# Kernel optimization log

Hardware: AMD Instinct MI355X
Metric: run time of the kernel (lower is better)

## Reference

```python
import jax, jax.numpy as jnp
import numpy as np

NUM_HEADS = 16
HEAD_DIM = 64
EMBED_DIM = 1024
NEG_INF = -1e9
LENGTHS = np.array([1024, 512, 768, 896, 1024, 640, 384, 896], dtype=np.int32)


def rotate_half(x):
    d = x.shape[-1] // 2
    return jnp.concatenate([-x[..., d:], x[..., :d]], axis=-1)


def setup_inputs() -> dict:
    key = jax.random.key(0)
    ks = jax.random.split(key, 8)
    E, H, Dh = EMBED_DIM, NUM_HEADS, HEAD_DIM
    T = int(LENGTHS.sum())  # 6144 packed tokens
    hidden_states = jax.random.normal(ks[0], (T, E), jnp.float32)
    # RoPE tables: positions restart at 0 for each packed segment
    pos = np.concatenate([np.arange(l) for l in LENGTHS]).astype(np.float32)
    inv_freq = 1.0 / (10000.0 ** (np.arange(0, Dh, 2, dtype=np.float32) / Dh))
    freqs = pos[:, None] * inv_freq[None, :]           # [T, Dh/2]
    emb = np.concatenate([freqs, freqs], axis=-1)       # [T, Dh]
    cos = jnp.asarray(np.cos(emb), jnp.float32)
    sin = jnp.asarray(np.sin(emb), jnp.float32)
    s = 0.02
    Wq = jax.random.normal(ks[1], (E, E), jnp.float32) * s
    Wk = jax.random.normal(ks[2], (E, E), jnp.float32) * s
    Wv = jax.random.normal(ks[3], (E, E), jnp.float32) * s
    Wo = jax.random.normal(ks[4], (E, E), jnp.float32) * s
    bq = jnp.zeros((E,), jnp.float32)
    bv = jnp.zeros((E,), jnp.float32)
    bo = jnp.zeros((E,), jnp.float32)
    return dict(hidden_states=hidden_states, seq_len=jnp.asarray(LENGTHS),
                cos=cos, sin=sin, Wq=Wq, bq=bq, Wk=Wk, Wv=Wv, bv=bv, Wo=Wo, bo=bo)


def reference(hidden_states, seq_len, cos, sin, Wq, bq, Wk, Wv, bv, Wo, bo):
    T, E = hidden_states.shape
    H, Dh = NUM_HEADS, HEAD_DIM
    # q/k/v projections (k_proj has no bias, matching nn.Linear(bias=False))
    q = (hidden_states @ Wq.T + bq).reshape(T, H, Dh)
    k = (hidden_states @ Wk.T).reshape(T, H, Dh)
    v = (hidden_states @ Wv.T + bv).reshape(T, H, Dh)
    # rotary embedding, cos/sin broadcast over heads
    c = cos[:, None, :]
    s = sin[:, None, :]
    q = q * c + rotate_half(q) * s
    k = k * c + rotate_half(k) * s
    # unpack ragged -> padded [B, Lmax, H, Dh] (indices are static wrt data)
    lens = np.asarray(seq_len)
    B = lens.shape[0]
    Lmax = int(lens.max())
    cu = np.concatenate([[0], np.cumsum(lens)])
    pad_idx = cu[:-1, None] + np.arange(Lmax)[None, :]   # [B, Lmax]
    valid = np.arange(Lmax)[None, :] < lens[:, None]     # [B, Lmax]
    pad_idx = np.where(valid, pad_idx, 0)
    qp = q[pad_idx]  # [B, Lmax, H, Dh]
    kp = k[pad_idx]
    vp = v[pad_idx]
    # attention with causal + key-padding mask (equivalent to per-segment loop)
    scores = jnp.einsum('bqhd,bkhd->bhqk', qp, kp) / np.sqrt(Dh).astype(np.float32)
    causal = np.tril(np.ones((Lmax, Lmax), dtype=bool))
    mask = causal[None, None, :, :] & valid[:, None, None, :]
    scores = jnp.where(mask, scores, NEG_INF)
    probs = jax.nn.softmax(scores, axis=-1)
    out = jnp.einsum('bhqk,bkhd->bqhd', probs, vp).reshape(B, Lmax, E)
    # repack padded -> [T, E]
    b_ids = np.repeat(np.arange(B), lens)
    l_ids = np.concatenate([np.arange(l) for l in lens])
    packed = out[b_ids, l_ids]
    return packed @ Wo.T + bo
```

## Files before the change

### kernel.cpp

```cpp
#include <hip/hip_runtime.h>
#include <stdint.h>

typedef __bf16 bf16;
typedef __bf16 bf16x8 __attribute__((ext_vector_type(8)));
typedef __bf16 bf16x4 __attribute__((ext_vector_type(4)));
typedef float f32x4 __attribute__((ext_vector_type(4)));

#define T_TOT 6144
#define E_DIM 1024
#define NHEAD 16

__device__ __forceinline__ void gload16(const void* g, void* l) {
    __builtin_amdgcn_global_load_lds((const __attribute__((address_space(1))) void*)g,
                                     (__attribute__((address_space(3))) void*)l, 16, 0, 0);
}

__global__ __launch_bounds__(256) void cvt_all_kernel(const float* __restrict__ hs,
        const float* __restrict__ wq, const float* __restrict__ wk,
        const float* __restrict__ wv, const float* __restrict__ wo,
        bf16* __restrict__ hsb, bf16* __restrict__ wqb, bf16* __restrict__ wkb,
        bf16* __restrict__ wvb, bf16* __restrict__ wob) {
    const size_t TE = (size_t)T_TOT * E_DIM;
    const size_t EE = (size_t)E_DIM * E_DIM;
    size_t i = ((size_t)blockIdx.x * 256 + threadIdx.x) * 4;
    const float* src; bf16* dst; size_t off;
    if (i < TE)               { src = hs; dst = hsb; off = i; }
    else if (i < TE + EE)     { src = wq; dst = wqb; off = i - TE; }
    else if (i < TE + 2 * EE) { src = wk; dst = wkb; off = i - TE - EE; }
    else if (i < TE + 3 * EE) { src = wv; dst = wvb; off = i - TE - 2 * EE; }
    else                      { src = wo; dst = wob; off = i - TE - 3 * EE; }
    float4 v = *reinterpret_cast<const float4*>(src + off);
    union { bf16 h[4]; uint2 u; } pk;
    pk.h[0] = (bf16)v.x; pk.h[1] = (bf16)v.y; pk.h[2] = (bf16)v.z; pk.h[3] = (bf16)v.w;
    *reinterpret_cast<uint2*>(dst + off) = pk.u;
}

__global__ __launch_bounds__(256, 2) void qkv_gemm_kernel(
        const bf16* __restrict__ hsb,
        const bf16* __restrict__ wq, const bf16* __restrict__ wk, const bf16* __restrict__ wv,
        const float* __restrict__ bq, const float* __restrict__ bv,
        const float* __restrict__ cosb, const float* __restrict__ sinb,
        bf16* __restrict__ qo, bf16* __restrict__ ko, bf16* __restrict__ vto) {
    __shared__ bf16 As[192 * 64];
    __shared__ bf16 Bs[128 * 64];

    const int b    = blockIdx.x;
    const int swzi = (b & 7) * 96 + (b >> 3);
    const int bn   = swzi & 7;
    const int t1   = swzi >> 3;
    const int bm   = t1 & 31;
    const int z    = t1 >> 5;
    const bf16*  W    = (z == 0) ? wq : (z == 1) ? wk : wv;
    const float* bias = (z == 0) ? bq : (z == 1) ? nullptr : bv;

    const int tid  = threadIdx.x;
    const int lane = tid & 63;
    const int wid  = tid >> 6;
    const int l15  = lane & 15, l4 = lane >> 4;
    const int wr   = wid >> 1, wc = wid & 1;

    f32x4 acc[6][4] = {};

    const bf16* Ag = hsb + (size_t)bm * 192 * E_DIM;
    const bf16* Bg = W   + (size_t)bn * 128 * E_DIM;

    const int srow = tid >> 3, sc8 = (tid & 7) * 8;

    for (int k0 = 0; k0 < E_DIM; k0 += 64) {
        #pragma unroll
        for (int j = 0; j < 6; ++j)
            gload16(Ag + (size_t)(j * 32 + srow) * E_DIM + k0 + sc8,
                    As + (size_t)(j * 256 + wid * 64) * 8);
        #pragma unroll
        for (int j = 0; j < 4; ++j)
            gload16(Bg + (size_t)(j * 32 + srow) * E_DIM + k0 + sc8,
                    Bs + (size_t)(j * 256 + wid * 64) * 8);
        __syncthreads();

        bf16x8 bfr[4][2];
        #pragma unroll
        for (int n = 0; n < 4; ++n)
            #pragma unroll
            for (int ks = 0; ks < 2; ++ks)
                bfr[n][ks] = *reinterpret_cast<const bf16x8*>(
                    &Bs[(wc * 64 + n * 16 + l15) * 64 + (ks * 4 + l4) * 8]);
        #pragma unroll
        for (int m = 0; m < 6; ++m) {
            bf16x8 af0 = *reinterpret_cast<const bf16x8*>(
                &As[(wr * 96 + m * 16 + l15) * 64 + l4 * 8]);
            bf16x8 af1 = *reinterpret_cast<const bf16x8*>(
                &As[(wr * 96 + m * 16 + l15) * 64 + (4 + l4) * 8]);
            #pragma unroll
            for (int n = 0; n < 4; ++n) {
                acc[m][n] = __builtin_amdgcn_mfma_f32_16x16x32_bf16(af0, bfr[n][0], acc[m][n], 0, 0, 0);
                acc[m][n] = __builtin_amdgcn_mfma_f32_16x16x32_bf16(af1, bfr[n][1], acc[m][n], 0, 0, 0);
            }
        }
        __syncthreads();
    }

    const int colb = bn * 128 + wc * 64;
    if (z <= 1) {
        bf16* out = (z == 0) ? qo : ko;
        #pragma unroll
        for (int n = 0; n < 2; ++n) {
            const int col_lo = colb + n * 16 + l15;
            const int dlo    = n * 16 + l15;
            const float b_lo = bias ? bias[col_lo] : 0.0f;
            const float b_hi = bias ? bias[col_lo + 32] : 0.0f;
            #pragma unroll
            for (int m = 0; m < 6; ++m) {
                #pragma unroll
                for (int r = 0; r < 4; ++r) {
                    const int t = bm * 192 + wr * 96 + m * 16 + l4 * 4 + r;
                    const float c = cosb[t * 64 + dlo];
                    const float s = sinb[t * 64 + dlo];
                    const float lo = acc[m][n][r] + b_lo;
                    const float hi = acc[m][n + 2][r] + b_hi;
                    out[(size_t)t * E_DIM + col_lo]      = (bf16)(lo * c - hi * s);
                    out[(size_t)t * E_DIM + col_lo + 32] = (bf16)(hi * c + lo * s);
                }
            }
        }
    } else {
        #pragma unroll
        for (int n = 0; n < 4; ++n) {
            const int col  = colb + n * 16 + l15;
            const float bc = bias[col];
            #pragma unroll
            for (int m = 0; m < 6; ++m) {
                const int t0r = bm * 192 + wr * 96 + m * 16 + l4 * 4;
                bf16x4 pk;
                #pragma unroll
                for (int r = 0; r < 4; ++r)
                    pk[r] = (bf16)(acc[m][n][r] + bc);
                *reinterpret_cast<bf16x4*>(vto + (size_t)col * T_TOT + t0r) = pk;
            }
        }
    }
}

__global__ __launch_bounds__(256, 4) void out_gemm_kernel(
        const bf16* __restrict__ attnb, const bf16* __restrict__ wo,
        const float* __restrict__ bo, float* __restrict__ out) {
    __shared__ bf16 As[64 * 64];
    __shared__ bf16 Bs[128 * 64];
    const int b   = blockIdx.x;
    const int swz = (b & 7) * 96 + (b >> 3);
    const int bn  = swz & 7;
    const int bm  = swz >> 3;

    const int tid  = threadIdx.x;
    const int lane = tid & 63;
    const int wid  = tid >> 6;
    const int l15  = lane & 15, l4 = lane >> 4;
    const int wr   = wid >> 1, wc = wid & 1;

    f32x4 acc[2][4] = {};

    const bf16* Ag = attnb + (size_t)bm * 64 * E_DIM;
    const bf16* Bg = wo    + (size_t)bn * 128 * E_DIM;

    const int srow = tid >> 3, sc8 = (tid & 7) * 8;

    for (int k0 = 0; k0 < E_DIM; k0 += 64) {
        #pragma unroll
        for (int j = 0; j < 2; ++j)
            gload16(Ag + (size_t)(j * 32 + srow) * E_DIM + k0 + sc8,
                    As + (size_t)(j * 256 + wid * 64) * 8);
        #pragma unroll
        for (int j = 0; j < 4; ++j)
            gload16(Bg + (size_t)(j * 32 + srow) * E_DIM + k0 + sc8,
                    Bs + (size_t)(j * 256 + wid * 64) * 8);
        __syncthreads();

        bf16x8 bfr[4][2];
        #pragma unroll
        for (int n = 0; n < 4; ++n)
            #pragma unroll
            for (int ks = 0; ks < 2; ++ks)
                bfr[n][ks] = *reinterpret_cast<const bf16x8*>(
                    &Bs[(wc * 64 + n * 16 + l15) * 64 + (ks * 4 + l4) * 8]);
        #pragma unroll
        for (int m = 0; m < 2; ++m) {
            bf16x8 af0 = *reinterpret_cast<const bf16x8*>(
                &As[(wr * 32 + m * 16 + l15) * 64 + l4 * 8]);
            bf16x8 af1 = *reinterpret_cast<const bf16x8*>(
                &As[(wr * 32 + m * 16 + l15) * 64 + (4 + l4) * 8]);
            #pragma unroll
            for (int n = 0; n < 4; ++n) {
                acc[m][n] = __builtin_amdgcn_mfma_f32_16x16x32_bf16(af0, bfr[n][0], acc[m][n], 0, 0, 0);
                acc[m][n] = __builtin_amdgcn_mfma_f32_16x16x32_bf16(af1, bfr[n][1], acc[m][n], 0, 0, 0);
            }
        }
        __syncthreads();
    }

    #pragma unroll
    for (int n = 0; n < 4; ++n) {
        const int col  = bn * 128 + wc * 64 + n * 16 + l15;
        const float bc = bo[col];
        #pragma unroll
        for (int m = 0; m < 2; ++m) {
            const int rowb = bm * 64 + wr * 32 + m * 16 + l4 * 4;
            #pragma unroll
            for (int r = 0; r < 4; ++r)
                out[(size_t)(rowb + r) * E_DIM + col] = acc[m][n][r] + bc;
        }
    }
}

__device__ const int g_pair_b[48] = {
    0,6,0,6,0,6,0,1,0,1,0,1,0,1,0,5,4,5,4,5,4,5,4,5,
    4,2,4,2,4,2,4,2,3,2,3,2,3,7,3,7,3,7,3,7,3,7,7,7};
__device__ const int g_pair_j[48] = {
    0,2,1,1,2,0,3,3,4,2,5,1,6,0,7,4,0,3,1,2,2,1,3,0,
    4,5,5,4,6,3,7,2,0,1,1,0,2,6,3,5,4,4,5,3,6,2,0,1};

__device__ __forceinline__ void stage_kv(const bf16* __restrict__ kp, const bf16* __restrict__ vtp,
                                         bf16* kls, bf16* vls, int tok0, int h,
                                         int wid, int lane) {
    #pragma unroll
    for (int j = 0; j < 2; ++j) {
        const int c   = j * 256 + wid * 64 + lane;
        const int row = c >> 3;
        const int c8s = (c & 7) ^ (row & 7);
        gload16(kp  + (size_t)(tok0 + row) * E_DIM + h * 64 + c8s * 8,
                kls + (size_t)(j * 256 + wid * 64) * 8);
        gload16(vtp + (size_t)(h * 64 + row) * T_TOT + tok0 + c8s * 8,
                vls + (size_t)(j * 256 + wid * 64) * 8);
    }
}

__device__ __forceinline__ int swz(int j, int col8) {
    return j * 64 + ((col8 ^ (j & 7)) << 3);
}

__global__ __launch_bounds__(256, 3) void attn_kernel(const bf16* __restrict__ q,
                                                      const bf16* __restrict__ k,
                                                      const bf16* __restrict__ vt,
                                                      bf16* __restrict__ attn) {
    const int cu[9] = {0, 1024, 1536, 2304, 3200, 4224, 4864, 5248, 6144};
    __shared__ bf16 kls[2][64 * 64];
    __shared__ bf16 vls[2][64 * 64];
    __shared__ bf16 p_lds[4][16][72];
    const int h   = blockIdx.x & 15;
    const int pid = blockIdx.x >> 4;
    const int tid = threadIdx.x, lane = tid & 63, wid = tid >> 6;
    const int l15 = lane & 15, l4 = lane >> 4;

    const int b   = g_pair_b[pid];
    const int jlo = g_pair_j[pid];
    const int nq  = (cu[b + 1] - cu[b]) >> 6;

    #pragma unroll 1
    for (int pass = 0; pass < 2; ++pass) {
        const int j   = pass ? (nq - 1 - jlo) : jlo;
        const int q0  = cu[b] + j * 64 + wid * 16;
        const int nkt = j + 1;
        const int pq  = j * 64 + wid * 16 + l15;

        bf16x8 qf[2];
        #pragma unroll
        for (int kk = 0; kk < 2; ++kk) {
            bf16x8 raw = *reinterpret_cast<const bf16x8*>(
                q + (size_t)(q0 + l15) * E_DIM + h * 64 + kk * 32 + l4 * 8);
            #pragma unroll
            for (int e = 0; e < 8; ++e)
                qf[kk][e] = (bf16)((float)raw[e] * 0.125f);
        }

        f32x4 o[4] = {};
        float mcur = -1e30f, lcur = 0.0f;

        stage_kv(k, vt, kls[0], vls[0], cu[b], h, wid, lane);
        __syncthreads();

        for (int kt = 0; kt < nkt; ++kt) {
            const int cur = kt & 1;
            if (kt + 1 < nkt)
                stage_kv(k, vt, kls[cur ^ 1], vls[cur ^ 1], cu[b] + (kt + 1) * 64, h, wid, lane);

            const int j0 = kt * 64;
            const bool diag = (kt == nkt - 1);

            f32x4 s[4] = {};
            #pragma unroll
            for (int nt = 0; nt < 4; ++nt) {
                #pragma unroll
                for (int kk = 0; kk < 2; ++kk) {
                    bf16x8 kf = *reinterpret_cast<const bf16x8*>(&kls[cur][swz(nt * 16 + l15, kk * 4 + l4)]);
                    s[nt] = __builtin_amdgcn_mfma_f32_16x16x32_bf16(kf, qf[kk], s[nt], 0, 0, 0);
                }
            }

            float tmax = -1e30f;
            #pragma unroll
            for (int nt = 0; nt < 4; ++nt) {
                #pragma unroll
                for (int r = 0; r < 4; ++r) {
                    float sv = s[nt][r];
                    if (diag) {
                        const int kp = j0 + nt * 16 + l4 * 4 + r;
                        sv = (kp <= pq) ? sv : -1e30f;
                    }
                    s[nt][r] = sv;
                    tmax = fmaxf(tmax, sv);
                }
            }
            tmax = fmaxf(tmax, __shfl_xor(tmax, 16));
            tmax = fmaxf(tmax, __shfl_xor(tmax, 32));

            if (!__all(tmax <= mcur + 8.0f)) {
                const float mnew  = fmaxf(mcur, tmax);
                const float alpha = __expf(mcur - mnew);
                #pragma unroll
                for (int nt = 0; nt < 4; ++nt)
                    #pragma unroll
                    for (int r = 0; r < 4; ++r) o[nt][r] *= alpha;
                lcur *= alpha;
                mcur = mnew;
            }

            float rs = 0.0f;
            #pragma unroll
            for (int nt = 0; nt < 4; ++nt) {
                bf16x4 pk;
                #pragma unroll
                for (int r = 0; r < 4; ++r) {
                    float p = __expf(s[nt][r] - mcur);
                    rs += p;
                    pk[r] = (bf16)p;
                }
                *reinterpret_cast<bf16x4*>(&p_lds[wid][l15][nt * 16 + l4 * 4]) = pk;
            }
            rs += __shfl_xor(rs, 16);
            rs += __shfl_xor(rs, 32);
            lcur += rs;

            bf16x8 pf[2];
            #pragma unroll
            for (int kk = 0; kk < 2; ++kk)
                pf[kk] = *reinterpret_cast<const bf16x8*>(&p_lds[wid][l15][kk * 32 + l4 * 8]);

            #pragma unroll
            for (int nt = 0; nt < 4; ++nt) {
                #pragma unroll
                for (int kk = 0; kk < 2; ++kk) {
                    bf16x8 vf = *reinterpret_cast<const bf16x8*>(&vls[cur][swz(nt * 16 + l15, kk * 4 + l4)]);
                    o[nt] = __builtin_amdgcn_mfma_f32_16x16x32_bf16(vf, pf[kk], o[nt], 0, 0, 0);
                }
            }
            __syncthreads();
        }

        const float rinv = __builtin_amdgcn_rcpf(lcur);
        #pragma unroll
        for (int nt = 0; nt < 4; ++nt) {
            bf16x4 pk;
            #pragma unroll
            for (int r = 0; r < 4; ++r)
                pk[r] = (bf16)(o[nt][r] * rinv);
            *reinterpret_cast<bf16x4*>(
                attn + (size_t)(q0 + l15) * E_DIM + h * 64 + nt * 16 + l4 * 4) = pk;
        }
    }
}

extern "C" void kernel_launch(void* const* d_in, const int* in_sizes, int n_in,
                              void* d_out, int out_size, void* d_ws, size_t ws_size,
                              hipStream_t stream) {
    const float* hs   = (const float*)d_in[0];
    const float* cosb = (const float*)d_in[2];
    const float* sinb = (const float*)d_in[3];
    const float* Wq   = (const float*)d_in[4];
    const float* bq   = (const float*)d_in[5];
    const float* Wk   = (const float*)d_in[6];
    const float* Wv   = (const float*)d_in[7];
    const float* bv   = (const float*)d_in[8];
    const float* Wo   = (const float*)d_in[9];
    const float* bo   = (const float*)d_in[10];

    const size_t TE = (size_t)T_TOT * E_DIM;
    const size_t EE = (size_t)E_DIM * E_DIM;

    char* w = (char*)d_ws;
    bf16* hsb   = (bf16*)w; w += TE * 2;
    bf16* wqb   = (bf16*)w; w += EE * 2;
    bf16* wkb   = (bf16*)w; w += EE * 2;
    bf16* wvb   = (bf16*)w; w += EE * 2;
    bf16* wob   = (bf16*)w; w += EE * 2;
    bf16* qb    = (bf16*)w; w += TE * 2;
    bf16* kb    = (bf16*)w; w += TE * 2;
    bf16* vtb   = (bf16*)w; w += TE * 2;
    bf16* attnb = (bf16*)w; w += TE * 2;

    const int cvt_blocks = (int)((TE + 4 * EE) / 4 / 256);
    cvt_all_kernel<<<cvt_blocks, 256, 0, stream>>>(hs, Wq, Wk, Wv, Wo, hsb, wqb, wkb, wvb, wob);

    qkv_gemm_kernel<<<768, 256, 0, stream>>>(hsb, wqb, wkb, wvb, bq, bv, cosb, sinb, qb, kb, vtb);

    attn_kernel<<<768, 256, 0, stream>>>(qb, kb, vtb, attnb);

    out_gemm_kernel<<<768, 256, 0, stream>>>(attnb, wob, bo, (float*)d_out);
}
```

Baseline: 113.0 us.

## Merge paired query tiles into one KV sweep sharing staged K/V tiles

Previously each block processed its low and high query tiles in two sequential passes, staging K/V tiles twice for the overlapping prefix. Now both query tiles are processed in a single loop over KV tiles up to the high tile. The low tile's MFMAs and softmax are predicated off once past its diagonal. This halves K/V staging and barrier count for the shared prefix, at the cost of doubled register state (two accumulators, two Q fragments) that may pressure occupancy under launch_bounds(256,3).

```diff
diff --git a/kernel.cpp b/kernel.cpp
--- a/kernel.cpp
+++ b/kernel.cpp
@@ -243,7 +243,8 @@
     const int cu[9] = {0, 1024, 1536, 2304, 3200, 4224, 4864, 5248, 6144};
     __shared__ bf16 kls[2][64 * 64];
     __shared__ bf16 vls[2][64 * 64];
-    __shared__ bf16 p_lds[4][16][72];
+    __shared__ bf16 pA_lds[4][16][72];
+    __shared__ bf16 pB_lds[4][16][72];
     const int h   = blockIdx.x & 15;
     const int pid = blockIdx.x >> 4;
     const int tid = threadIdx.x, lane = tid & 63, wid = tid >> 6;
@@ -252,118 +253,133 @@
     const int b   = g_pair_b[pid];
     const int jlo = g_pair_j[pid];
     const int nq  = (cu[b + 1] - cu[b]) >> 6;
-
-    #pragma unroll 1
-    for (int pass = 0; pass < 2; ++pass) {
-        const int j   = pass ? (nq - 1 - jlo) : jlo;
-        const int q0  = cu[b] + j * 64 + wid * 16;
-        const int nkt = j + 1;
-        const int pq  = j * 64 + wid * 16 + l15;
-
-        bf16x8 qf[2];
-        #pragma unroll
-        for (int kk = 0; kk < 2; ++kk) {
-            bf16x8 raw = *reinterpret_cast<const bf16x8*>(
-                q + (size_t)(q0 + l15) * E_DIM + h * 64 + kk * 32 + l4 * 8);
-            #pragma unroll
-            for (int e = 0; e < 8; ++e)
-                qf[kk][e] = (bf16)((float)raw[e] * 0.125f);
-        }
-
-        f32x4 o[4] = {};
-        float mcur = -1e30f, lcur = 0.0f;
-
-        stage_kv(k, vt, kls[0], vls[0], cu[b], h, wid, lane);
-        __syncthreads();
-
-        for (int kt = 0; kt < nkt; ++kt) {
-            const int cur = kt & 1;
-            if (kt + 1 < nkt)
-                stage_kv(k, vt, kls[cur ^ 1], vls[cur ^ 1], cu[b] + (kt + 1) * 64, h, wid, lane);
-
-            const int j0 = kt * 64;
-            const bool diag = (kt == nkt - 1);
-
-            f32x4 s[4] = {};
-            #pragma unroll
-            for (int nt = 0; nt < 4; ++nt) {
+    const int jhi = nq - 1 - jlo;
+
+    const int qA0 = cu[b] + jlo * 64 + wid * 16;
+    const int qB0 = cu[b] + jhi * 64 + wid * 16;
+    const int pqA = jlo * 64 + wid * 16 + l15;
+    const int pqB = jhi * 64 + wid * 16 + l15;
+
+    bf16x8 qfA[2], qfB[2];
+    #pragma unroll
+    for (int kk = 0; kk < 2; ++kk) {
+        bf16x8 ra = *reinterpret_cast<const bf16x8*>(
+            q + (size_t)(qA0 + l15) * E_DIM + h * 64 + kk * 32 + l4 * 8);
+        bf16x8 rb = *reinterpret_cast<const bf16x8*>(
+            q + (size_t)(qB0 + l15) * E_DIM + h * 64 + kk * 32 + l4 * 8);
+        #pragma unroll
+        for (int e = 0; e < 8; ++e) {
+            qfA[kk][e] = (bf16)((float)ra[e] * 0.125f);
+            qfB[kk][e] = (bf16)((float)rb[e] * 0.125f);
+        }
+    }
+
+    f32x4 oA[4] = {}, oB[4] = {};
+    float mA = -1e30f, lA = 0.0f, mB = -1e30f, lB = 0.0f;
+
+    auto softmax_tile = [&](f32x4 (&s)[4], float& m, float& l, f32x4 (&o)[4],
+                            bf16 (*plds)[72], int pq, bool diag, int j0) {
+        float tmax = -1e30f;
+        #pragma unroll
+        for (int nt = 0; nt < 4; ++nt) {
+            #pragma unroll
+            for (int r = 0; r < 4; ++r) {
+                float sv = s[nt][r];
+                if (diag) {
+                    const int kp = j0 + nt * 16 + l4 * 4 + r;
+                    sv = (kp <= pq) ? sv : -1e30f;
+                }
+                s[nt][r] = sv;
+                tmax = fmaxf(tmax, sv);
+            }
+        }
+        tmax = fmaxf(tmax, __shfl_xor(tmax, 16));
+        tmax = fmaxf(tmax, __shfl_xor(tmax, 32));
+        if (!__all(tmax <= m + 8.0f)) {
+            const float mnew  = fmaxf(m, tmax);
+            const float alpha = __expf(m - mnew);
+            #pragma unroll
+            for (int nt = 0; nt < 4; ++nt)
                 #pragma unroll
-                for (int kk = 0; kk < 2; ++kk) {
-                    bf16x8 kf = *reinterpret_cast<const bf16x8*>(&kls[cur][swz(nt * 16 + l15, kk * 4 + l4)]);
-                    s[nt] = __builtin_amdgcn_mfma_f32_16x16x32_bf16(kf, qf[kk], s[nt], 0, 0, 0);
-                }
-            }
-
-            float tmax = -1e30f;
-            #pragma unroll
-            for (int nt = 0; nt < 4; ++nt) {
-                #pragma unroll
-                for (int r = 0; r < 4; ++r) {
-                    float sv = s[nt][r];
-                    if (diag) {
-                        const int kp = j0 + nt * 16 + l4 * 4 + r;
-                        sv = (kp <= pq) ? sv : -1e30f;
-                    }
-                    s[nt][r] = sv;
-                    tmax = fmaxf(tmax, sv);
-                }
-            }
-            tmax = fmaxf(tmax, __shfl_xor(tmax, 16));
-            tmax = fmaxf(tmax, __shfl_xor(tmax, 32));
-
-            if (!__all(tmax <= mcur + 8.0f)) {
-                const float mnew  = fmaxf(mcur, tmax);
-                const float alpha = __expf(mcur - mnew);
-                #pragma unroll
-                for (int nt = 0; nt < 4; ++nt)
-                    #pragma unroll
-                    for (int r = 0; r < 4; ++r) o[nt][r] *= alpha;
-                lcur *= alpha;
-                mcur = mnew;
-            }
-
-            float rs = 0.0f;
-            #pragma unroll
-            for (int nt = 0; nt < 4; ++nt) {
-                bf16x4 pk;
-                #pragma unroll
-                for (int r = 0; r < 4; ++r) {
-                    float p = __expf(s[nt][r] - mcur);
-                    rs += p;
-                    pk[r] = (bf16)p;
-                }
-                *reinterpret_cast<bf16x4*>(&p_lds[wid][l15][nt * 16 + l4 * 4]) = pk;
-            }
-            rs += __shfl_xor(rs, 16);
-            rs += __shfl_xor(rs, 32);
-            lcur += rs;
-
-            bf16x8 pf[2];
-            #pragma unroll
-            for (int kk = 0; kk < 2; ++kk)
-                pf[kk] = *reinterpret_cast<const bf16x8*>(&p_lds[wid][l15][kk * 32 + l4 * 8]);
-
-            #pragma unroll
-            for (int nt = 0; nt < 4; ++nt) {
-                #pragma unroll
-                for (int kk = 0; kk < 2; ++kk) {
-                    bf16x8 vf = *reinterpret_cast<const bf16x8*>(&vls[cur][swz(nt * 16 + l15, kk * 4 + l4)]);
-                    o[nt] = __builtin_amdgcn_mfma_f32_16x16x32_bf16(vf, pf[kk], o[nt], 0, 0, 0);
-                }
-            }
-            __syncthreads();
-        }
-
-        const float rinv = __builtin_amdgcn_rcpf(lcur);
+                for (int r = 0; r < 4; ++r) o[nt][r] *= alpha;
+            l *= alpha;
+            m = mnew;
+        }
+        float rs = 0.0f;
         #pragma unroll
         for (int nt = 0; nt < 4; ++nt) {
             bf16x4 pk;
             #pragma unroll
-            for (int r = 0; r < 4; ++r)
-                pk[r] = (bf16)(o[nt][r] * rinv);
-            *reinterpret_cast<bf16x4*>(
-                attn + (size_t)(q0 + l15) * E_DIM + h * 64 + nt * 16 + l4 * 4) = pk;
-        }
+            for (int r = 0; r < 4; ++r) {
+                float p = __expf(s[nt][r] - m);
+                rs += p;
+                pk[r] = (bf16)p;
+            }
+            *reinterpret_cast<bf16x4*>(&plds[l15][nt * 16 + l4 * 4]) = pk;
+        }
+        rs += __shfl_xor(rs, 16);
+        rs += __shfl_xor(rs, 32);
+        l += rs;
+    };
+
+    stage_kv(k, vt, kls[0], vls[0], cu[b], h, wid, lane);
+    __syncthreads();
+
+    const int nkt = jhi + 1;
+    for (int kt = 0; kt < nkt; ++kt) {
+        const int cur = kt & 1;
+        if (kt + 1 < nkt)
+            stage_kv(k, vt, kls[cur ^ 1], vls[cur ^ 1], cu[b] + (kt + 1) * 64, h, wid, lane);
+
+        const int j0   = kt * 64;
+        const bool actA = (kt <= jlo);
+
+        f32x4 sA[4] = {}, sB[4] = {};
+        #pragma unroll
+        for (int nt = 0; nt < 4; ++nt) {
+            #pragma unroll
+            for (int kk = 0; kk < 2; ++kk) {
+                bf16x8 kf = *reinterpret_cast<const bf16x8*>(&kls[cur][swz(nt * 16 + l15, kk * 4 + l4)]);
+                if (actA) sA[nt] = __builtin_amdgcn_mfma_f32_16x16x32_bf16(kf, qfA[kk], sA[nt], 0, 0, 0);
+                sB[nt] = __builtin_amdgcn_mfma_f32_16x16x32_bf16(kf, qfB[kk], sB[nt], 0, 0, 0);
+            }
+        }
+
+        if (actA) softmax_tile(sA, mA, lA, oA, pA_lds[wid], pqA, kt == jlo, j0);
+        softmax_tile(sB, mB, lB, oB, pB_lds[wid], pqB, kt == jhi, j0);
+
+        bf16x8 pfA[2], pfB[2];
+        #pragma unroll
+        for (int kk = 0; kk < 2; ++kk) {
+            if (actA) pfA[kk] = *reinterpret_cast<const bf16x8*>(&pA_lds[wid][l15][kk * 32 + l4 * 8]);
+            pfB[kk] = *reinterpret_cast<const bf16x8*>(&pB_lds[wid][l15][kk * 32 + l4 * 8]);
+        }
+        #pragma unroll
+        for (int nt = 0; nt < 4; ++nt) {
+            #pragma unroll
+            for (int kk = 0; kk < 2; ++kk) {
+                bf16x8 vf = *reinterpret_cast<const bf16x8*>(&vls[cur][swz(nt * 16 + l15, kk * 4 + l4)]);
+                if (actA) oA[nt] = __builtin_amdgcn_mfma_f32_16x16x32_bf16(vf, pfA[kk], oA[nt], 0, 0, 0);
+                oB[nt] = __builtin_amdgcn_mfma_f32_16x16x32_bf16(vf, pfB[kk], oB[nt], 0, 0, 0);
+            }
+        }
+        __syncthreads();
+    }
+
+    const float rinvA = __builtin_amdgcn_rcpf(lA);
+    const float rinvB = __builtin_amdgcn_rcpf(lB);
+    #pragma unroll
+    for (int nt = 0; nt < 4; ++nt) {
+        bf16x4 pa, pb;
+        #pragma unroll
+        for (int r = 0; r < 4; ++r) {
+            pa[r] = (bf16)(oA[nt][r] * rinvA);
+            pb[r] = (bf16)(oB[nt][r] * rinvB);
+        }
+        *reinterpret_cast<bf16x4*>(
+            attn + (size_t)(qA0 + l15) * E_DIM + h * 64 + nt * 16 + l4 * 4) = pa;
+        *reinterpret_cast<bf16x4*>(
+            attn + (size_t)(qB0 + l15) * E_DIM + h * 64 + nt * 16 + l4 * 4) = pb;
     }
 }
 
```

Result: slower. 117.4 us (+3.9%).
